# Performance work log

Hardware: AMD Instinct MI355X
Metric: run time of the kernel (lower is better)

Reference implementation:

```python
import jax, jax.numpy as jnp
import numpy as np

WS = (7, 7, 7)          # window size (S, H, W)
DIM = 192
HEADS = 6
BW = 256                # B_ = batch * num_windows
N = WS[0] * WS[1] * WS[2]  # 343 tokens per window


def _relative_position_index(ws):
    # Faithful reproduction of the torch buffer construction.
    coords = np.stack(np.meshgrid(np.arange(ws[0]), np.arange(ws[1]), np.arange(ws[2]), indexing='ij'))
    flat = coords.reshape(3, -1)                      # [3, N]
    rel = flat[:, :, None] - flat[:, None, :]         # [3, N, N]
    rel = rel.transpose(1, 2, 0).astype(np.int32)     # [N, N, 3]
    rel[..., 0] += ws[0] - 1
    rel[..., 1] += ws[1] - 1
    rel[..., 2] += ws[2] - 1
    rel[..., 0] *= (2 * ws[1] - 1) * (2 * ws[2] - 1)
    rel[..., 1] *= 2 * ws[2] - 1
    return rel.sum(-1)                                # [N, N] in [0, (2ws-1)^3)


def setup_inputs() -> dict:
    key = jax.random.key(0)
    ks = jax.random.split(key, 6)
    table_size = (2 * WS[0] - 1) * (2 * WS[1] - 1) * (2 * WS[2] - 1)  # 2197
    return {
        'x': jax.random.normal(ks[0], (BW, N, DIM), dtype=jnp.float32),
        'w_qkv': jax.random.normal(ks[1], (3 * DIM, DIM), dtype=jnp.float32) * 0.02,
        'b_qkv': jnp.zeros((3 * DIM,), dtype=jnp.float32),
        'w_proj': jax.random.normal(ks[2], (DIM, DIM), dtype=jnp.float32) * 0.02,
        'b_proj': jnp.zeros((DIM,), dtype=jnp.float32),
        'bias_table': jax.random.normal(ks[3], (table_size, HEADS), dtype=jnp.float32) * 0.02,
        'rel_index': jnp.asarray(_relative_position_index(WS)),  # [N, N] int32
        'is_global': 0,
    }


def reference(x, w_qkv, b_qkv, w_proj, b_proj, bias_table, rel_index, is_global):
    # x: [B_, N, C]; dropout rates are 0 (eval), is_global=0 -> local window path.
    B_, n, C = x.shape
    H = HEADS
    hd = C // H
    scale = jnp.asarray(hd, x.dtype) ** -0.5

    qkv = x @ w_qkv.T + b_qkv                         # [B_, N, 3C]
    qkv = qkv.reshape(B_, n, 3, H, hd)
    q = qkv[:, :, 0].transpose(0, 2, 1, 3) * scale    # [B_, H, N, hd]
    k = qkv[:, :, 1].transpose(0, 2, 1, 3)
    v = qkv[:, :, 2].transpose(0, 2, 1, 3)

    attn = jnp.einsum('bhqd,bhkd->bhqk', q, k)        # [B_, H, N, N]
    bias = bias_table[rel_index]                      # gather: [N, N, H]
    attn = attn + bias.transpose(2, 0, 1)[None]       # add per-head relative bias
    attn = jax.nn.softmax(attn, axis=-1)

    out = jnp.einsum('bhqk,bhkd->bhqd', attn, v)      # [B_, H, N, hd]
    out = out.transpose(0, 2, 1, 3).reshape(B_, n, C)
    return out @ w_proj.T + b_proj                    # [B_, N, C]
```

## Files before the change

### kernel.cpp

```cpp
#include <hip/hip_runtime.h>
#include <hip/hip_bf16.h>

#define BWIN 256
#define NTOK 343
#define CDIM 192
#define NH   6
#define HD   32
#define QKVF 576
#define NROWS (BWIN * NTOK)
#define SCALE 0.17677669529663687f
#define LOG2E 1.4426950408889634f

typedef unsigned short u16;
typedef unsigned int   u32;
typedef short bf16x8 __attribute__((ext_vector_type(8)));
typedef float f32x4 __attribute__((ext_vector_type(4)));

#define OFF_QKVB 0UL
#define OFF_OPB  101154816UL
#define OFF_WQB  134873088UL
#define OFF_WPB  135094272UL
#define OFF_BQS  135168000UL
#define OFF_BMB  135170304UL
#define WS_NEED  136619136UL

__device__ __forceinline__ u16 f2bf(float f) {
    u32 u = __float_as_uint(f);
    u += 0x7FFFu + ((u >> 16) & 1u);
    return (u16)(u >> 16);
}
__device__ __forceinline__ float bf2f(u16 h) {
    return __uint_as_float(((u32)h) << 16);
}
__device__ __forceinline__ u32 pk2bf(float a, float b) {
    union { __hip_bfloat162 h; u32 u; } v;
    v.h = __float22bfloat162_rn(make_float2(a, b));
    return v.u;
}

__global__ void ws_too_small_sentinel(float* out) { out[0] = 1.0e6f; }

__global__ __launch_bounds__(256) void cvt_small(
    const float* __restrict__ wq, const float* __restrict__ wp,
    const float* __restrict__ bq, const float* __restrict__ btab,
    const int* __restrict__ ridx,
    u16* __restrict__ wqb, u16* __restrict__ wpb,
    float* __restrict__ bqs, u16* __restrict__ bmb)
{
    const int i = blockIdx.x * 256 + threadIdx.x;
    if (i < 110592) {
        const int f = i / 192;
        wqb[i] = f2bf(wq[i] * (f < CDIM ? SCALE * LOG2E : 1.0f));
    } else if (i < 147456) {
        wpb[i - 110592] = f2bf(wp[i - 110592]);
    } else if (i < 148032) {
        const int f = i - 147456;
        bqs[f] = bq[f] * (f < CDIM ? SCALE * LOG2E : 1.0f);
    } else if (i < 872448) {
        const int u = i - 148032;
        const int hh = u / 120736;
        const int rem = u - hh * 120736;
        const int q = rem / 352;
        const int j = rem - q * 352;
        const float v = (j < NTOK) ? btab[ridx[q * NTOK + j] * NH + hh] * LOG2E
                                   : -10000.0f;
        bmb[(hh * NTOK + q) * 352 + j] = f2bf(v);
    }
}

__global__ __launch_bounds__(256, 3) void gemm_qkv(
    const float* __restrict__ x, const u16* __restrict__ wqb,
    const float* __restrict__ bqs, u16* __restrict__ qkvb)
{
    __shared__ __align__(16) u16 smem[128 * 200];
    u16* Xs = smem;
    u16* Ct = smem;
    const int f0 = blockIdx.x * 96, m0 = blockIdx.y * 128;
    const int tid = threadIdx.x;
    const int wave = tid >> 6, lane = tid & 63, g = lane >> 4, cl = lane & 15;
    const int wm = (wave >> 1) * 64, wf = (wave & 1) * 48;

    #pragma unroll
    for (int p = 0; p < 24; ++p) {
        const int u = tid + 256 * p;
        const int row = u / 48, c = u - row * 48;
        const float4 v = *(const float4*)(x + (size_t)(m0 + row) * CDIM + c * 4);
        *(uint2*)(Xs + row * 200 + c * 4) = make_uint2(pk2bf(v.x, v.y), pk2bf(v.z, v.w));
    }
    __syncthreads();

    f32x4 acc[4][3];
    #pragma unroll
    for (int t = 0; t < 4; ++t)
        #pragma unroll
        for (int s = 0; s < 3; ++s) acc[t][s] = (f32x4){0.f, 0.f, 0.f, 0.f};

    const u16* wbase = wqb + (size_t)(f0 + wf + cl) * CDIM + g * 8;
    #pragma unroll
    for (int kk = 0; kk < 6; ++kk) {
        const int kcol = kk * 32;
        bf16x8 a[4], bb[3];
        #pragma unroll
        for (int s = 0; s < 3; ++s)
            bb[s] = *(const bf16x8*)(wbase + (size_t)(s * 16) * CDIM + kcol);
        #pragma unroll
        for (int t = 0; t < 4; ++t)
            a[t] = *(const bf16x8*)(Xs + (wm + t * 16 + cl) * 200 + kcol + g * 8);
        #pragma unroll
        for (int t = 0; t < 4; ++t)
            #pragma unroll
            for (int s = 0; s < 3; ++s)
                acc[t][s] = __builtin_amdgcn_mfma_f32_16x16x32_bf16(a[t], bb[s], acc[t][s], 0, 0, 0);
    }

    __syncthreads();
    #pragma unroll
    for (int s = 0; s < 3; ++s) {
        const float bv = bqs[f0 + wf + s * 16 + cl];
        #pragma unroll
        for (int t = 0; t < 4; ++t) {
            const int row = wm + t * 16 + g * 4;
            const int col = wf + s * 16 + cl;
            const u32 p01 = pk2bf(acc[t][s][0] + bv, acc[t][s][1] + bv);
            const u32 p23 = pk2bf(acc[t][s][2] + bv, acc[t][s][3] + bv);
            Ct[(row + 0) * 104 + col] = (u16)p01;
            Ct[(row + 1) * 104 + col] = (u16)(p01 >> 16);
            Ct[(row + 2) * 104 + col] = (u16)p23;
            Ct[(row + 3) * 104 + col] = (u16)(p23 >> 16);
        }
    }
    __syncthreads();
    #pragma unroll
    for (int p = 0; p < 6; ++p) {
        const int u = tid + 256 * p;
        const int row = u / 12, c = u - row * 12;
        *(float4*)(qkvb + (size_t)(m0 + row) * QKVF + f0 + c * 8) =
            *(const float4*)(Ct + row * 104 + c * 8);
    }
}

__global__ __launch_bounds__(256, 4) void attn_mfma(
    const u16* __restrict__ qkvb, const u16* __restrict__ bmb,
    u16* __restrict__ opb)
{
    __shared__ u16 Vt[HD][360];
    __shared__ u16 Os[4][16][32];
    const int b = blockIdx.x, h = blockIdx.y;
    const int tid = threadIdx.x;
    const int wave = tid >> 6, lane = tid & 63, g = lane >> 4, cl = lane & 15;
    const size_t rowbase = (size_t)b * NTOK;

    for (int u = tid; u < 1408; u += 256) {
        const int row = u >> 2, seg = u & 3;
        union { float4 f; u16 hx[8]; } vv;
        vv.f = make_float4(0.f, 0.f, 0.f, 0.f);
        if (row < NTOK)
            vv.f = *(const float4*)(qkvb + (rowbase + row) * QKVF + 2 * CDIM + h * HD + seg * 8);
        const int jl = row & 31;
        const int slot = (jl < 16) ? ((jl >> 2) << 3) + (jl & 3)
                                   : (((jl - 16) >> 2) << 3) + 4 + (jl & 3);
        const int pcol = (row & ~31) + slot;
        #pragma unroll
        for (int e = 0; e < 8; ++e) Vt[seg * 8 + e][pcol] = vv.hx[e];
    }
    __syncthreads();

    bf16x8 ones;
    #pragma unroll
    for (int e = 0; e < 8; ++e) ones[e] = (short)0x3F80;

    for (int base = wave * 2; base < 22; base += 8) {
        const int q0a = base * 16, q0b = q0a + 16;
        const bf16x8 qa0 = *(const bf16x8*)(qkvb + (rowbase + min(q0a + cl, NTOK - 1)) * QKVF + h * HD + g * 8);
        const bf16x8 qa1 = *(const bf16x8*)(qkvb + (rowbase + min(q0b + cl, NTOK - 1)) * QKVF + h * HD + g * 8);
        const u16* browA = bmb + ((size_t)h * NTOK + min(q0a + cl, NTOK - 1)) * 352;
        const u16* browB = bmb + ((size_t)h * NTOK + min(q0b + cl, NTOK - 1)) * 352;

        bf16x8 kb0 = *(const bf16x8*)(qkvb + (rowbase + cl) * QKVF + CDIM + h * HD + g * 8);
        bf16x8 kb1 = *(const bf16x8*)(qkvb + (rowbase + 16 + cl) * QKVF + CDIM + h * HD + g * 8);
        ushort4 bA0 = *(const ushort4*)(browA + g * 4);
        ushort4 bA1 = *(const ushort4*)(browA + 16 + g * 4);
        ushort4 bB0 = *(const ushort4*)(browB + g * 4);
        ushort4 bB1 = *(const ushort4*)(browB + 16 + g * 4);

        f32x4 oA0 = {0,0,0,0}, oA1 = {0,0,0,0}, lA = {0,0,0,0};
        f32x4 oB0 = {0,0,0,0}, oB1 = {0,0,0,0}, lB = {0,0,0,0};

        for (int jc = 0; jc < 11; ++jc) {
            const int j0 = jc * 32;
            const bf16x8 ck0 = kb0, ck1 = kb1;
            const ushort4 cA0 = bA0, cA1 = bA1, cB0 = bB0, cB1 = bB1;
            if (jc < 10) {
                const int jn = j0 + 32;
                kb0 = *(const bf16x8*)(qkvb + (rowbase + min(jn + cl, NTOK - 1)) * QKVF + CDIM + h * HD + g * 8);
                kb1 = *(const bf16x8*)(qkvb + (rowbase + min(jn + 16 + cl, NTOK - 1)) * QKVF + CDIM + h * HD + g * 8);
                bA0 = *(const ushort4*)(browA + jn + g * 4);
                bA1 = *(const ushort4*)(browA + jn + 16 + g * 4);
                bB0 = *(const ushort4*)(browB + jn + g * 4);
                bB1 = *(const ushort4*)(browB + jn + 16 + g * 4);
            }
            const bf16x8 vb0 = *(const bf16x8*)&Vt[cl][j0 + g * 8];
            const bf16x8 vb1 = *(const bf16x8*)&Vt[16 + cl][j0 + g * 8];

            {
                f32x4 c0 = { bf2f(cA0.x), bf2f(cA0.y), bf2f(cA0.z), bf2f(cA0.w) };
                f32x4 c1 = { bf2f(cA1.x), bf2f(cA1.y), bf2f(cA1.z), bf2f(cA1.w) };
                const f32x4 s0 = __builtin_amdgcn_mfma_f32_16x16x32_bf16(ck0, qa0, c0, 0, 0, 0);
                const f32x4 s1 = __builtin_amdgcn_mfma_f32_16x16x32_bf16(ck1, qa0, c1, 0, 0, 0);
                union { bf16x8 v; u32 w[4]; } pa;
                pa.w[0] = pk2bf(__builtin_amdgcn_exp2f(s0[0]), __builtin_amdgcn_exp2f(s0[1]));
                pa.w[1] = pk2bf(__builtin_amdgcn_exp2f(s0[2]), __builtin_amdgcn_exp2f(s0[3]));
                pa.w[2] = pk2bf(__builtin_amdgcn_exp2f(s1[0]), __builtin_amdgcn_exp2f(s1[1]));
                pa.w[3] = pk2bf(__builtin_amdgcn_exp2f(s1[2]), __builtin_amdgcn_exp2f(s1[3]));
                oA0 = __builtin_amdgcn_mfma_f32_16x16x32_bf16(pa.v, vb0, oA0, 0, 0, 0);
                oA1 = __builtin_amdgcn_mfma_f32_16x16x32_bf16(pa.v, vb1, oA1, 0, 0, 0);
                lA  = __builtin_amdgcn_mfma_f32_16x16x32_bf16(pa.v, ones, lA, 0, 0, 0);
            }
            {
                f32x4 c0 = { bf2f(cB0.x), bf2f(cB0.y), bf2f(cB0.z), bf2f(cB0.w) };
                f32x4 c1 = { bf2f(cB1.x), bf2f(cB1.y), bf2f(cB1.z), bf2f(cB1.w) };
                const f32x4 s0 = __builtin_amdgcn_mfma_f32_16x16x32_bf16(ck0, qa1, c0, 0, 0, 0);
                const f32x4 s1 = __builtin_amdgcn_mfma_f32_16x16x32_bf16(ck1, qa1, c1, 0, 0, 0);
                union { bf16x8 v; u32 w[4]; } pa;
                pa.w[0] = pk2bf(__builtin_amdgcn_exp2f(s0[0]), __builtin_amdgcn_exp2f(s0[1]));
                pa.w[1] = pk2bf(__builtin_amdgcn_exp2f(s0[2]), __builtin_amdgcn_exp2f(s0[3]));
                pa.w[2] = pk2bf(__builtin_amdgcn_exp2f(s1[0]), __builtin_amdgcn_exp2f(s1[1]));
                pa.w[3] = pk2bf(__builtin_amdgcn_exp2f(s1[2]), __builtin_amdgcn_exp2f(s1[3]));
                oB0 = __builtin_amdgcn_mfma_f32_16x16x32_bf16(pa.v, vb0, oB0, 0, 0, 0);
                oB1 = __builtin_amdgcn_mfma_f32_16x16x32_bf16(pa.v, vb1, oB1, 0, 0, 0);
                lB  = __builtin_amdgcn_mfma_f32_16x16x32_bf16(pa.v, ones, lB, 0, 0, 0);
            }
        }
        #pragma unroll
        for (int half = 0; half < 2; ++half) {
            const f32x4 o0 = half ? oB0 : oA0;
            const f32x4 o1 = half ? oB1 : oA1;
            const f32x4 lc = half ? lB : lA;
            const int q0 = half ? q0b : q0a;
            #pragma unroll
            for (int r = 0; r < 4; ++r) {
                const float inv = 1.0f / lc[r];
                Os[wave][g * 4 + r][cl]      = f2bf(o0[r] * inv);
                Os[wave][g * 4 + r][16 + cl] = f2bf(o1[r] * inv);
            }
            const int row = lane >> 2, cg = (lane & 3) * 8;
            const int q = q0 + row;
            if (q < NTOK)
                *(float4*)(opb + (rowbase + q) * CDIM + h * HD + cg) =
                    *(const float4*)&Os[wave][row][cg];
        }
    }
}

__global__ __launch_bounds__(256, 3) void gemm_proj(
    const u16* __restrict__ opb, const u16* __restrict__ wpb,
    const float* __restrict__ bp, float* __restrict__ out)
{
    __shared__ __align__(16) u16 smem[128 * 200];
    u16*   Xs = smem;
    float* Cf = (float*)smem;
    const int f0 = blockIdx.x * 96, m0 = blockIdx.y * 128;
    const int tid = threadIdx.x;
    const int wave = tid >> 6, lane = tid & 63, g = lane >> 4, cl = lane & 15;
    const int wm = (wave >> 1) * 64, wf = (wave & 1) * 48;

    #pragma unroll
    for (int p = 0; p < 12; ++p) {
        const int u = tid + 256 * p;
        const int row = u / 24, c = u - row * 24;
        *(float4*)(Xs + row * 200 + c * 8) =
            *(const float4*)(opb + (size_t)(m0 + row) * CDIM + c * 8);
    }
    __syncthreads();

    f32x4 acc[4][3];
    #pragma unroll
    for (int t = 0; t < 4; ++t)
        #pragma unroll
        for (int s = 0; s < 3; ++s) acc[t][s] = (f32x4){0.f, 0.f, 0.f, 0.f};

    const u16* wbase = wpb + (size_t)(f0 + wf + cl) * CDIM + g * 8;
    #pragma unroll
    for (int kk = 0; kk < 6; ++kk) {
        const int kcol = kk * 32;
        bf16x8 a[4], bb[3];
        #pragma unroll
        for (int s = 0; s < 3; ++s)
            bb[s] = *(const bf16x8*)(wbase + (size_t)(s * 16) * CDIM + kcol);
        #pragma unroll
        for (int t = 0; t < 4; ++t)
            a[t] = *(const bf16x8*)(Xs + (wm + t * 16 + cl) * 200 + kcol + g * 8);
        #pragma unroll
        for (int t = 0; t < 4; ++t)
            #pragma unroll
            for (int s = 0; s < 3; ++s)
                acc[t][s] = __builtin_amdgcn_mfma_f32_16x16x32_bf16(a[t], bb[s], acc[t][s], 0, 0, 0);
    }

    #pragma unroll
    for (int half = 0; half < 2; ++half) {
        __syncthreads();
        if ((wave >> 1) == half) {
            #pragma unroll
            for (int s = 0; s < 3; ++s) {
                const float bv = bp[f0 + wf + s * 16 + cl];
                #pragma unroll
                for (int t = 0; t < 4; ++t)
                    #pragma unroll
                    for (int r = 0; r < 4; ++r)
                        Cf[(t * 16 + g * 4 + r) * 104 + wf + s * 16 + cl] = acc[t][s][r] + bv;
            }
        }
        __syncthreads();
        #pragma unroll
        for (int p = 0; p < 6; ++p) {
            const int u = tid + 256 * p;
            const int row = u / 24, c = u - row * 24;
            *(float4*)(out + (size_t)(m0 + half * 64 + row) * CDIM + f0 + c * 4) =
                *(const float4*)(Cf + row * 104 + c * 4);
        }
    }
}

extern "C" void kernel_launch(void* const* d_in, const int* in_sizes, int n_in,
                              void* d_out, int out_size, void* d_ws, size_t ws_size,
                              hipStream_t stream) {
    const float* x     = (const float*)d_in[0];
    const float* wqkv  = (const float*)d_in[1];
    const float* bqkv  = (const float*)d_in[2];
    const float* wproj = (const float*)d_in[3];
    const float* bproj = (const float*)d_in[4];
    const float* btab  = (const float*)d_in[5];
    const int*   ridx  = (const int*)d_in[6];
    float* out = (float*)d_out;

    if (ws_size < WS_NEED) {
        hipLaunchKernelGGL(ws_too_small_sentinel, dim3(1), dim3(1), 0, stream, out);
        return;
    }
    char* ws = (char*)d_ws;
    u16*   qkvb = (u16*)(ws + OFF_QKVB);
    u16*   opb  = (u16*)(ws + OFF_OPB);
    u16*   wqb  = (u16*)(ws + OFF_WQB);
    u16*   wpb  = (u16*)(ws + OFF_WPB);
    float* bqs  = (float*)(ws + OFF_BQS);
    u16*   bmb  = (u16*)(ws + OFF_BMB);

    hipLaunchKernelGGL(cvt_small, dim3(3408), dim3(256), 0, stream,
                       wqkv, wproj, bqkv, btab, ridx, wqb, wpb, bqs, bmb);
    hipLaunchKernelGGL(gemm_qkv, dim3(6, NROWS / 128), dim3(256), 0, stream,
                       x, wqb, bqs, qkvb);
    hipLaunchKernelGGL(attn_mfma, dim3(BWIN, NH), dim3(256), 0, stream,
                       qkvb, bmb, opb);
    hipLaunchKernelGGL(gemm_proj, dim3(2, NROWS / 128), dim3(256), 0, stream,
                       opb, wpb, bproj, out);
}
```

Before: 315.9 us.

## Write attention output in place into QKV buffer and pad tails to drop clamps

The attention kernel now writes its per-head output into the Q columns of the QKV workspace instead of a separate output buffer, and the projection GEMM reads that strided region. K, Q and bias rows are padded (zeroed extra QKV rows, a 352x352 bias matrix) so the per-load min() clamps disappear. Attention launch bounds rise to 6 blocks per CU and the V^T shared row stride shrinks to 352. This aims to cut address arithmetic and workspace footprint and raise occupancy, at the risk of more LDS bank conflicts from the 352 stride and less efficient strided reads in the projection GEMM.

Measured after the change: 341.7 us. 8.2% more time.

```diff
diff --git a/kernel.cpp b/kernel.cpp
--- a/kernel.cpp
+++ b/kernel.cpp
@@ -8,6 +8,8 @@
 #define HD   32
 #define QKVF 576
 #define NROWS (BWIN * NTOK)
+#define NPAD  16
+#define BQ    352
 #define SCALE 0.17677669529663687f
 #define LOG2E 1.4426950408889634f
 
@@ -17,12 +19,11 @@
 typedef float f32x4 __attribute__((ext_vector_type(4)));
 
 #define OFF_QKVB 0UL
-#define OFF_OPB  101154816UL
-#define OFF_WQB  134873088UL
-#define OFF_WPB  135094272UL
-#define OFF_BQS  135168000UL
-#define OFF_BMB  135170304UL
-#define WS_NEED  136619136UL
+#define OFF_WQB  101173248UL
+#define OFF_WPB  101394432UL
+#define OFF_BQS  101468160UL
+#define OFF_BMB  101470464UL
+#define WS_NEED  102957312UL
 
 __device__ __forceinline__ u16 f2bf(float f) {
     u32 u = __float_as_uint(f);
@@ -45,7 +46,7 @@
     const float* __restrict__ bq, const float* __restrict__ btab,
     const int* __restrict__ ridx,
     u16* __restrict__ wqb, u16* __restrict__ wpb,
-    float* __restrict__ bqs, u16* __restrict__ bmb)
+    float* __restrict__ bqs, u16* __restrict__ bmb, u16* __restrict__ qkvb)
 {
     const int i = blockIdx.x * 256 + threadIdx.x;
     if (i < 110592) {
@@ -56,15 +57,19 @@
     } else if (i < 148032) {
         const int f = i - 147456;
         bqs[f] = bq[f] * (f < CDIM ? SCALE * LOG2E : 1.0f);
-    } else if (i < 872448) {
+    } else if (i < 891456) {
         const int u = i - 148032;
-        const int hh = u / 120736;
-        const int rem = u - hh * 120736;
-        const int q = rem / 352;
-        const int j = rem - q * 352;
-        const float v = (j < NTOK) ? btab[ridx[q * NTOK + j] * NH + hh] * LOG2E
-                                   : -10000.0f;
-        bmb[(hh * NTOK + q) * 352 + j] = f2bf(v);
+        const int hh = u / 123904;
+        const int rem = u - hh * 123904;
+        const int q = rem / BQ;
+        const int j = rem - q * BQ;
+        const float v = (j >= NTOK) ? -10000.0f
+                      : (q >= NTOK) ? 0.0f
+                      : btab[ridx[q * NTOK + j] * NH + hh] * LOG2E;
+        bmb[(hh * BQ + q) * BQ + j] = f2bf(v);
+    } else if (i < 896064) {
+        const int t = i - 891456;
+        ((u32*)qkvb)[87808u * 288u + t] = 0u;
     }
 }
 
@@ -139,16 +144,17 @@
     }
 }
 
-__global__ __launch_bounds__(256, 4) void attn_mfma(
-    const u16* __restrict__ qkvb, const u16* __restrict__ bmb,
-    u16* __restrict__ opb)
+__global__ __launch_bounds__(256, 6) void attn_mfma(
+    u16* __restrict__ qkvb, const u16* __restrict__ bmb)
 {
-    __shared__ u16 Vt[HD][360];
+    __shared__ u16 Vt[HD][352];
     __shared__ u16 Os[4][16][32];
     const int b = blockIdx.x, h = blockIdx.y;
     const int tid = threadIdx.x;
     const int wave = tid >> 6, lane = tid & 63, g = lane >> 4, cl = lane & 15;
     const size_t rowbase = (size_t)b * NTOK;
+    const u16* __restrict__ qptr = qkvb + rowbase * QKVF + h * HD;
+    const u16* __restrict__ kptr = qptr + CDIM;
 
     for (int u = tid; u < 1408; u += 256) {
         const int row = u >> 2, seg = u & 3;
@@ -171,13 +177,13 @@
 
     for (int base = wave * 2; base < 22; base += 8) {
         const int q0a = base * 16, q0b = q0a + 16;
-        const bf16x8 qa0 = *(const bf16x8*)(qkvb + (rowbase + min(q0a + cl, NTOK - 1)) * QKVF + h * HD + g * 8);
-        const bf16x8 qa1 = *(const bf16x8*)(qkvb + (rowbase + min(q0b + cl, NTOK - 1)) * QKVF + h * HD + g * 8);
-        const u16* browA = bmb + ((size_t)h * NTOK + min(q0a + cl, NTOK - 1)) * 352;
-        const u16* browB = bmb + ((size_t)h * NTOK + min(q0b + cl, NTOK - 1)) * 352;
-
-        bf16x8 kb0 = *(const bf16x8*)(qkvb + (rowbase + cl) * QKVF + CDIM + h * HD + g * 8);
-        bf16x8 kb1 = *(const bf16x8*)(qkvb + (rowbase + 16 + cl) * QKVF + CDIM + h * HD + g * 8);
+        const bf16x8 qa0 = *(const bf16x8*)(qptr + (size_t)(q0a + cl) * QKVF + g * 8);
+        const bf16x8 qa1 = *(const bf16x8*)(qptr + (size_t)(q0b + cl) * QKVF + g * 8);
+        const u16* browA = bmb + ((size_t)h * BQ + q0a + cl) * BQ;
+        const u16* browB = browA + (size_t)16 * BQ;
+
+        bf16x8 kb0 = *(const bf16x8*)(kptr + (size_t)cl * QKVF + g * 8);
+        bf16x8 kb1 = *(const bf16x8*)(kptr + (size_t)(16 + cl) * QKVF + g * 8);
         ushort4 bA0 = *(const ushort4*)(browA + g * 4);
         ushort4 bA1 = *(const ushort4*)(browA + 16 + g * 4);
         ushort4 bB0 = *(const ushort4*)(browB + g * 4);
@@ -192,8 +198,8 @@
             const ushort4 cA0 = bA0, cA1 = bA1, cB0 = bB0, cB1 = bB1;
             if (jc < 10) {
                 const int jn = j0 + 32;
-                kb0 = *(const bf16x8*)(qkvb + (rowbase + min(jn + cl, NTOK - 1)) * QKVF + CDIM + h * HD + g * 8);
-                kb1 = *(const bf16x8*)(qkvb + (rowbase + min(jn + 16 + cl, NTOK - 1)) * QKVF + CDIM + h * HD + g * 8);
+                kb0 = *(const bf16x8*)(kptr + (size_t)(jn + cl) * QKVF + g * 8);
+                kb1 = *(const bf16x8*)(kptr + (size_t)(jn + 16 + cl) * QKVF + g * 8);
                 bA0 = *(const ushort4*)(browA + jn + g * 4);
                 bA1 = *(const ushort4*)(browA + jn + 16 + g * 4);
                 bB0 = *(const ushort4*)(browB + jn + g * 4);
@@ -246,7 +252,7 @@
             const int row = lane >> 2, cg = (lane & 3) * 8;
             const int q = q0 + row;
             if (q < NTOK)
-                *(float4*)(opb + (rowbase + q) * CDIM + h * HD + cg) =
+                *(float4*)(qkvb + (rowbase + q) * QKVF + h * HD + cg) =
                     *(const float4*)&Os[wave][row][cg];
         }
     }
@@ -269,7 +275,7 @@
         const int u = tid + 256 * p;
         const int row = u / 24, c = u - row * 24;
         *(float4*)(Xs + row * 200 + c * 8) =
-            *(const float4*)(opb + (size_t)(m0 + row) * CDIM + c * 8);
+            *(const float4*)(opb + (size_t)(m0 + row) * QKVF + c * 8);
     }
     __syncthreads();
 
@@ -340,18 +346,17 @@
     }
     char* ws = (char*)d_ws;
     u16*   qkvb = (u16*)(ws + OFF_QKVB);
-    u16*   opb  = (u16*)(ws + OFF_OPB);
     u16*   wqb  = (u16*)(ws + OFF_WQB);
     u16*   wpb  = (u16*)(ws + OFF_WPB);
     float* bqs  = (float*)(ws + OFF_BQS);
     u16*   bmb  = (u16*)(ws + OFF_BMB);
 
-    hipLaunchKernelGGL(cvt_small, dim3(3408), dim3(256), 0, stream,
-                       wqkv, wproj, bqkv, btab, ridx, wqb, wpb, bqs, bmb);
+    hipLaunchKernelGGL(cvt_small, dim3(3501), dim3(256), 0, stream,
+                       wqkv, wproj, bqkv, btab, ridx, wqb, wpb, bqs, bmb, qkvb);
     hipLaunchKernelGGL(gemm_qkv, dim3(6, NROWS / 128), dim3(256), 0, stream,
                        x, wqb, bqs, qkvb);
     hipLaunchKernelGGL(attn_mfma, dim3(BWIN, NH), dim3(256), 0, stream,
-                       qkvb, bmb, opb);
+                       qkvb, bmb);
     hipLaunchKernelGGL(gemm_proj, dim3(2, NROWS / 128), dim3(256), 0, stream,
-                       opb, wpb, bproj, out);
-}
+                       qkvb, wpb, bproj, out);
+}
```
